# Optimization experiments

Measured on AMD Instinct MI355X. Metric: run time of the kernel, lower is better.

The kernel has to match this reference:

```python
import jax, jax.numpy as jnp
import numpy as np
from functools import partial

T = 2048        # num tokens
H = 2048        # hidden_size
I = 1024        # intermediate_size (per TP rank)
E = 8           # num_local_experts
TOP_K = 2       # num_experts_per_tok


def setup_inputs() -> dict:
    key = jax.random.key(0)
    k1, k2, k3, k4 = jax.random.split(key, 4)
    hidden_states = jax.random.normal(k1, (T, H), dtype=jnp.float32)
    gate_w = jax.random.normal(k2, (E, H), dtype=jnp.float32) * (H ** -0.5)
    # ws: [E, 2I, H] merged w1(gate)+w3(up); w2s: [E, H, I]
    ws = jax.random.normal(k3, (E, 2 * I, H), dtype=jnp.float32) * (H ** -0.5)
    w2s = jax.random.normal(k4, (E, H, I), dtype=jnp.float32) * (I ** -0.5)
    return {"hidden_states": hidden_states, "gate_w": gate_w, "ws": ws, "w2s": w2s}


def _moe_forward(x, gate_w, ws, w2s):
    num_tokens = x.shape[0]
    # router: replicated linear -> softmax -> top-k (fused_topk semantics)
    router_logits = x @ gate_w.T                     # [T, E]
    probs = jax.nn.softmax(router_logits, axis=-1)
    topk_weights, topk_ids = jax.lax.top_k(probs, TOP_K)   # [T, K]
    if TOP_K > 1:  # renormalize (do_normalize = top_k > 1)
        topk_weights = topk_weights / jnp.sum(topk_weights, axis=-1, keepdims=True)
    # combine weights as dense [T, E] (zero where expert not selected)
    cw = jnp.zeros((num_tokens, E), dtype=x.dtype)
    cw = cw.at[jnp.arange(num_tokens)[:, None], topk_ids].add(topk_weights)
    # grouped expert GEMMs; loop over the small fixed expert set
    out = jnp.zeros_like(x)
    for e in range(E):
        gate_up = x @ ws[e].T                        # [T, 2I]
        act = jax.nn.silu(gate_up[:, :I]) * gate_up[:, I:]  # SiluAndMul
        out = out + cw[:, e:e + 1] * (act @ w2s[e].T)       # [T, H]
    return out


def reference(hidden_states, gate_w, ws, w2s):
    return _moe_forward(hidden_states, gate_w, ws, w2s)
```

## Files before the change

### kernel.cpp

```cpp
#include <hip/hip_runtime.h>
#include <hip/hip_bf16.h>
#include <stdint.h>

#define TOKS  2048
#define HID   2048
#define ITR   1024
#define NEXP  8
#define NROWS 4096

typedef __attribute__((ext_vector_type(4))) float f32x4;
typedef __attribute__((ext_vector_type(8))) __bf16 bf16x8;
typedef __attribute__((ext_vector_type(8))) unsigned short u16x8;
typedef __attribute__((ext_vector_type(4))) unsigned short u16x4;

__device__ __forceinline__ unsigned short f2bf(float f) {
    union { float f; uint32_t u; } c; c.f = f;
    return (unsigned short)((c.u + 0x7FFFu + ((c.u >> 16) & 1u)) >> 16);
}

__device__ __forceinline__ void gll16(const unsigned short* g, unsigned short* l) {
    __builtin_amdgcn_global_load_lds(
        (const __attribute__((address_space(1))) unsigned int*)g,
        (__attribute__((address_space(3))) unsigned int*)l,
        16, 0, 0);
}

__global__ __launch_bounds__(256) void prep_kernel(const float* __restrict__ ws,
                                                   const float* __restrict__ w2s,
                                                   const float* __restrict__ x,
                                                   const float* __restrict__ gw,
                                                   float* __restrict__ out,
                                                   unsigned short* __restrict__ da,
                                                   unsigned short* __restrict__ db,
                                                   unsigned short* __restrict__ xb,
                                                   int* __restrict__ topk_id,
                                                   float* __restrict__ topk_w) {
    const int tid = threadIdx.x;

    if (tid < 64) {
        const int t = blockIdx.x;
        const int lane = tid;
        float acc[NEXP];
#pragma unroll
        for (int e = 0; e < NEXP; ++e) acc[e] = 0.f;
        const float* xr = x + (size_t)t * HID;
        unsigned short* xbr = xb + (size_t)t * HID;
        for (int s4 = lane; s4 < HID / 4; s4 += 64) {
            const f32x4 xv = *(const f32x4*)(xr + s4 * 4);
            u16x4 o;
#pragma unroll
            for (int j = 0; j < 4; ++j) o[j] = f2bf(xv[j]);
            *(u16x4*)(xbr + s4 * 4) = o;
#pragma unroll
            for (int e = 0; e < NEXP; ++e) {
                const f32x4 gv = *(const f32x4*)(gw + e * HID + s4 * 4);
                acc[e] += xv[0] * gv[0] + xv[1] * gv[1] + xv[2] * gv[2] + xv[3] * gv[3];
            }
        }
#pragma unroll
        for (int e = 0; e < NEXP; ++e) {
            float v = acc[e];
            for (int off = 32; off > 0; off >>= 1) v += __shfl_down(v, off, 64);
            acc[e] = v;
        }
        if (lane == 0) {
            float m0 = -1e30f, m1 = -1e30f; int i0 = 0, i1 = 0;
#pragma unroll
            for (int e = 0; e < NEXP; ++e) {
                float v = acc[e];
                if (v > m0) { m1 = m0; i1 = i0; m0 = v; i0 = e; }
                else if (v > m1) { m1 = v; i1 = e; }
            }
            float w0 = 1.f / (1.f + expf(m1 - m0));
            topk_id[t * 2] = i0; topk_id[t * 2 + 1] = i1;
            topk_w[t * 2] = w0;  topk_w[t * 2 + 1] = 1.f - w0;
        }
    }

    const int NA = (NEXP * 2 * ITR * HID) / 16;
    const int NB = (NEXP * HID * ITR) / 16;
    const int NO = (TOKS * HID) / 16;
    const int i0 = blockIdx.x * 256 + tid;
    const int stride = gridDim.x * 256;
    for (int k = i0; k < NA; k += stride) {
        const f32x4* p = (const f32x4*)(ws + (size_t)k * 16);
        f32x4 a = p[0], b = p[1], c = p[2], d = p[3];
        u16x8 o0, o1;
#pragma unroll
        for (int j = 0; j < 4; ++j) { o0[j] = f2bf(a[j]); o0[4 + j] = f2bf(b[j]); }
#pragma unroll
        for (int j = 0; j < 4; ++j) { o1[j] = f2bf(c[j]); o1[4 + j] = f2bf(d[j]); }
        *(u16x8*)(da + (size_t)k * 16) = o0;
        *(u16x8*)(da + (size_t)k * 16 + 8) = o1;
    }
    for (int k = i0; k < NB; k += stride) {
        const f32x4* p = (const f32x4*)(w2s + (size_t)k * 16);
        f32x4 a = p[0], b = p[1], c = p[2], d = p[3];
        u16x8 o0, o1;
#pragma unroll
        for (int j = 0; j < 4; ++j) { o0[j] = f2bf(a[j]); o0[4 + j] = f2bf(b[j]); }
#pragma unroll
        for (int j = 0; j < 4; ++j) { o1[j] = f2bf(c[j]); o1[4 + j] = f2bf(d[j]); }
        *(u16x8*)(db + (size_t)k * 16) = o0;
        *(u16x8*)(db + (size_t)k * 16 + 8) = o1;
    }
    const f32x4 z = (f32x4){0.f, 0.f, 0.f, 0.f};
    for (int k = i0; k < NO; k += stride) {
        f32x4* q = (f32x4*)(out + (size_t)k * 16);
        q[0] = z; q[1] = z; q[2] = z; q[3] = z;
    }
}

__global__ __launch_bounds__(512) void sort_kernel(const int* __restrict__ topk_id,
                                                   const float* __restrict__ topk_w,
                                                   int* __restrict__ sorted_tok,
                                                   float* __restrict__ row_w,
                                                   int* __restrict__ offsets,
                                                   int* __restrict__ counts) {
    __shared__ int sc[512 * NEXP];
    __shared__ int base[NEXP + 1];
    const int t = threadIdx.x;
    int ids[8];
    int* myrow = &sc[t * NEXP];
#pragma unroll
    for (int e = 0; e < NEXP; ++e) myrow[e] = 0;
#pragma unroll
    for (int j = 0; j < 8; ++j) { ids[j] = topk_id[t * 8 + j]; myrow[ids[j]]++; }
    __syncthreads();
    for (int d = 1; d < 512; d <<= 1) {
        int add[NEXP];
        const bool act = (t >= d);
#pragma unroll
        for (int e = 0; e < NEXP; ++e) add[e] = act ? sc[(t - d) * NEXP + e] : 0;
        __syncthreads();
        if (act) {
#pragma unroll
            for (int e = 0; e < NEXP; ++e) sc[t * NEXP + e] += add[e];
        }
        __syncthreads();
    }
    if (t == 0) {
        int s = 0;
        for (int e = 0; e < NEXP; ++e) {
            const int tot = sc[511 * NEXP + e];
            base[e] = s; offsets[e] = s; counts[e] = tot; s += tot;
        }
        base[NEXP] = s; offsets[NEXP] = s;
    }
    __syncthreads();
    int own[NEXP];
#pragma unroll
    for (int e = 0; e < NEXP; ++e) {
        int c = 0;
#pragma unroll
        for (int j = 0; j < 8; ++j) c += (ids[j] == e) ? 1 : 0;
        own[e] = c;
    }
#pragma unroll
    for (int e = 0; e < NEXP; ++e) myrow[e] = base[e] + myrow[e] - own[e];
#pragma unroll
    for (int j = 0; j < 8; ++j) {
        const int p = t * 8 + j;
        const int pos = myrow[ids[j]]++;
        sorted_tok[pos] = p >> 1;
        row_w[pos] = topk_w[p];
    }
}

__global__ __launch_bounds__(512) void gemm1_kernel(const unsigned short* __restrict__ Wb,
                                                    const unsigned short* __restrict__ Xb,
                                                    const int* __restrict__ offsets,
                                                    const int* __restrict__ counts,
                                                    const int* __restrict__ sorted_tok,
                                                    unsigned short* __restrict__ act) {
    const int b = blockIdx.x;
    const int e = b & 7;
    const int r = b >> 3;
    const int mt = r >> 4;
    const int nt = r & 15;
    const int cnt = counts[e];
    if (mt * 128 >= cnt) return;
    const int offs = offsets[e];
    const int tid = threadIdx.x, lane = tid & 63, wid = tid >> 6;
    const int wr = wid >> 2, wc = wid & 3;

    __shared__ unsigned short sA[3][128 * 32];
    __shared__ unsigned short sB[3][128 * 32];

    const int srow = tid >> 2;
    const int swz = (((tid & 3) ^ (srow & 3))) * 8;
    int ar = mt * 128 + srow;
    if (ar >= cnt) ar = cnt - 1;
    const int tok = sorted_tok[offs + ar];
    const unsigned short* aSrc = Xb + (size_t)tok * HID + swz;
    const unsigned short* wBase = Wb + (size_t)e * (2 * ITR) * HID;
    const int wrow = (srow < 64) ? (nt * 64 + srow) : (ITR + nt * 64 + (srow - 64));
    const unsigned short* bSrc = wBase + (size_t)wrow * HID + swz;
    const int ldsOff = wid * 16 * 32;

    f32x4 accg[4], accu[4];
#pragma unroll
    for (int i = 0; i < 4; ++i) {
        accg[i] = (f32x4){0.f, 0.f, 0.f, 0.f};
        accu[i] = (f32x4){0.f, 0.f, 0.f, 0.f};
    }

#define G1_STAGE(ks) do {                                  \
        const int k0_ = (ks) * 32;                         \
        gll16(aSrc + k0_, sA[(ks) % 3] + ldsOff);          \
        gll16(bSrc + k0_, sB[(ks) % 3] + ldsOff);          \
    } while (0)

    G1_STAGE(0);
    G1_STAGE(1);

    const int fr = lane & 15, fq = lane >> 4;
    const int sfo = (fq ^ (fr & 3)) * 8;
    const int NS = HID / 32;
    for (int ks = 0; ks < NS; ++ks) {
        const int cur = ks % 3;
        if (ks == NS - 1) asm volatile("s_waitcnt vmcnt(0)" ::: "memory");
        else              asm volatile("s_waitcnt vmcnt(2)" ::: "memory");
        __builtin_amdgcn_s_barrier();
        asm volatile("" ::: "memory");
        if (ks + 2 < NS) G1_STAGE(ks + 2);
        bf16x8 af[4], bg, bu;
#pragma unroll
        for (int mi = 0; mi < 4; ++mi)
            af[mi] = *(const bf16x8*)&sA[cur][(wr * 64 + mi * 16 + fr) * 32 + sfo];
        bg = *(const bf16x8*)&sB[cur][(wc * 16 + fr) * 32 + sfo];
        bu = *(const bf16x8*)&sB[cur][(64 + wc * 16 + fr) * 32 + sfo];
        __builtin_amdgcn_s_setprio(1);
#pragma unroll
        for (int mi = 0; mi < 4; ++mi) {
            accg[mi] = __builtin_amdgcn_mfma_f32_16x16x32_bf16(af[mi], bg, accg[mi], 0, 0, 0);
            accu[mi] = __builtin_amdgcn_mfma_f32_16x16x32_bf16(af[mi], bu, accu[mi], 0, 0, 0);
        }
        __builtin_amdgcn_s_setprio(0);
        asm volatile("" ::: "memory");
    }
#undef G1_STAGE

#pragma unroll
    for (int mi = 0; mi < 4; ++mi) {
#pragma unroll
        for (int j = 0; j < 4; ++j) {
            const int gr = mt * 128 + wr * 64 + mi * 16 + fq * 4 + j;
            if (gr < cnt) {
                const float g = accg[mi][j], u = accu[mi][j];
                const float s = g / (1.f + expf(-g));
                act[(size_t)(offs + gr) * ITR + nt * 64 + wc * 16 + fr] = f2bf(s * u);
            }
        }
    }
}

__global__ __launch_bounds__(512) void gemm2_kernel(const unsigned short* __restrict__ W2b,
                                                    const unsigned short* __restrict__ actb,
                                                    const int* __restrict__ offsets,
                                                    const int* __restrict__ counts,
                                                    const int* __restrict__ sorted_tok,
                                                    const float* __restrict__ row_w,
                                                    float* __restrict__ out) {
    const int b = blockIdx.x;
    const int e = b & 7;
    const int r = b >> 3;
    const int mt = r >> 4;
    const int nt = r & 15;
    const int cnt = counts[e];
    if (mt * 128 >= cnt) return;
    const int offs = offsets[e];
    const int tid = threadIdx.x, lane = tid & 63, wid = tid >> 6;
    const int wr = wid >> 2, wc = wid & 3;

    __shared__ unsigned short sA[3][128 * 32];
    __shared__ unsigned short sB[3][128 * 32];

    const int srow = tid >> 2;
    const int swz = (((tid & 3) ^ (srow & 3))) * 8;
    int ar = mt * 128 + srow;
    if (ar >= cnt) ar = cnt - 1;
    const unsigned short* aSrc = actb + (size_t)(offs + ar) * ITR + swz;
    const unsigned short* bSrc = W2b + ((size_t)e * HID + nt * 128 + srow) * ITR + swz;
    const int ldsOff = wid * 16 * 32;

    f32x4 acc[4][2];
#pragma unroll
    for (int i = 0; i < 4; ++i)
#pragma unroll
        for (int j = 0; j < 2; ++j) acc[i][j] = (f32x4){0.f, 0.f, 0.f, 0.f};

#define G2_STAGE(ks) do {                                  \
        const int k0_ = (ks) * 32;                         \
        gll16(aSrc + k0_, sA[(ks) % 3] + ldsOff);          \
        gll16(bSrc + k0_, sB[(ks) % 3] + ldsOff);          \
    } while (0)

    G2_STAGE(0);
    G2_STAGE(1);

    const int fr = lane & 15, fq = lane >> 4;
    const int sfo = (fq ^ (fr & 3)) * 8;
    const int NS = ITR / 32;
    for (int ks = 0; ks < NS; ++ks) {
        const int cur = ks % 3;
        if (ks == NS - 1) asm volatile("s_waitcnt vmcnt(0)" ::: "memory");
        else              asm volatile("s_waitcnt vmcnt(2)" ::: "memory");
        __builtin_amdgcn_s_barrier();
        asm volatile("" ::: "memory");
        if (ks + 2 < NS) G2_STAGE(ks + 2);
        bf16x8 af[4], bfv[2];
#pragma unroll
        for (int mi = 0; mi < 4; ++mi)
            af[mi] = *(const bf16x8*)&sA[cur][(wr * 64 + mi * 16 + fr) * 32 + sfo];
#pragma unroll
        for (int ni = 0; ni < 2; ++ni)
            bfv[ni] = *(const bf16x8*)&sB[cur][(wc * 32 + ni * 16 + fr) * 32 + sfo];
        __builtin_amdgcn_s_setprio(1);
#pragma unroll
        for (int mi = 0; mi < 4; ++mi)
#pragma unroll
            for (int ni = 0; ni < 2; ++ni)
                acc[mi][ni] = __builtin_amdgcn_mfma_f32_16x16x32_bf16(af[mi], bfv[ni], acc[mi][ni], 0, 0, 0);
        __builtin_amdgcn_s_setprio(0);
        asm volatile("" ::: "memory");
    }
#undef G2_STAGE

#pragma unroll
    for (int mi = 0; mi < 4; ++mi) {
#pragma unroll
        for (int j = 0; j < 4; ++j) {
            const int gr = mt * 128 + wr * 64 + mi * 16 + fq * 4 + j;
            if (gr < cnt) {
                const int pos = offs + gr;
                const int t = sorted_tok[pos];
                const float w = row_w[pos];
#pragma unroll
                for (int ni = 0; ni < 2; ++ni) {
                    const int col = nt * 128 + wc * 32 + ni * 16 + fr;
                    atomicAdd(&out[(size_t)t * HID + col], w * acc[mi][ni][j]);
                }
            }
        }
    }
}

extern "C" void kernel_launch(void* const* d_in, const int* in_sizes, int n_in,
                              void* d_out, int out_size, void* d_ws, size_t ws_size,
                              hipStream_t stream) {
    const float* x   = (const float*)d_in[0];
    const float* gw  = (const float*)d_in[1];
    const float* ws  = (const float*)d_in[2];
    const float* w2s = (const float*)d_in[3];
    float* out = (float*)d_out;

    char* wsb = (char*)d_ws;
    int*   counts     = (int*)(wsb + 0);
    int*   offsets    = (int*)(wsb + 256);
    int*   topk_id    = (int*)(wsb + 4096);
    float* topk_w     = (float*)(wsb + 20480);
    int*   sorted_tok = (int*)(wsb + 36864);
    float* row_w      = (float*)(wsb + 53248);
    unsigned short* xb    = (unsigned short*)(wsb + (1u << 20));
    unsigned short* actb  = (unsigned short*)(wsb + 9437184);
    unsigned short* wsb16 = (unsigned short*)(wsb + 17825792);
    unsigned short* w2b   = (unsigned short*)(wsb + 84934656);

    prep_kernel<<<2048, 256, 0, stream>>>(ws, w2s, x, gw, out, wsb16, w2b, xb, topk_id, topk_w);
    sort_kernel<<<1, 512, 0, stream>>>(topk_id, topk_w, sorted_tok, row_w, offsets, counts);
    gemm1_kernel<<<2048, 512, 0, stream>>>(wsb16, xb, offsets, counts, sorted_tok, actb);
    gemm2_kernel<<<2048, 512, 0, stream>>>(w2b, actb, offsets, counts, sorted_tok, row_w, out);
}
```

Before: 186.7 us.

## Move w2 bf16 conversion into idle gemm1 blocks and memset output

```diff
diff --git a/kernel.cpp b/kernel.cpp
--- a/kernel.cpp
+++ b/kernel.cpp
@@ -26,12 +26,9 @@
 }
 
 __global__ __launch_bounds__(256) void prep_kernel(const float* __restrict__ ws,
-                                                   const float* __restrict__ w2s,
                                                    const float* __restrict__ x,
                                                    const float* __restrict__ gw,
-                                                   float* __restrict__ out,
                                                    unsigned short* __restrict__ da,
-                                                   unsigned short* __restrict__ db,
                                                    unsigned short* __restrict__ xb,
                                                    int* __restrict__ topk_id,
                                                    float* __restrict__ topk_w) {
@@ -78,8 +75,6 @@
     }
 
     const int NA = (NEXP * 2 * ITR * HID) / 16;
-    const int NB = (NEXP * HID * ITR) / 16;
-    const int NO = (TOKS * HID) / 16;
     const int i0 = blockIdx.x * 256 + tid;
     const int stride = gridDim.x * 256;
     for (int k = i0; k < NA; k += stride) {
@@ -92,22 +87,6 @@
         for (int j = 0; j < 4; ++j) { o1[j] = f2bf(c[j]); o1[4 + j] = f2bf(d[j]); }
         *(u16x8*)(da + (size_t)k * 16) = o0;
         *(u16x8*)(da + (size_t)k * 16 + 8) = o1;
-    }
-    for (int k = i0; k < NB; k += stride) {
-        const f32x4* p = (const f32x4*)(w2s + (size_t)k * 16);
-        f32x4 a = p[0], b = p[1], c = p[2], d = p[3];
-        u16x8 o0, o1;
-#pragma unroll
-        for (int j = 0; j < 4; ++j) { o0[j] = f2bf(a[j]); o0[4 + j] = f2bf(b[j]); }
-#pragma unroll
-        for (int j = 0; j < 4; ++j) { o1[j] = f2bf(c[j]); o1[4 + j] = f2bf(d[j]); }
-        *(u16x8*)(db + (size_t)k * 16) = o0;
-        *(u16x8*)(db + (size_t)k * 16 + 8) = o1;
-    }
-    const f32x4 z = (f32x4){0.f, 0.f, 0.f, 0.f};
-    for (int k = i0; k < NO; k += stride) {
-        f32x4* q = (f32x4*)(out + (size_t)k * 16);
-        q[0] = z; q[1] = z; q[2] = z; q[3] = z;
     }
 }
 
@@ -169,6 +148,8 @@
 
 __global__ __launch_bounds__(512) void gemm1_kernel(const unsigned short* __restrict__ Wb,
                                                     const unsigned short* __restrict__ Xb,
+                                                    const float* __restrict__ w2s,
+                                                    unsigned short* __restrict__ w2b,
                                                     const int* __restrict__ offsets,
                                                     const int* __restrict__ counts,
                                                     const int* __restrict__ sorted_tok,
@@ -176,12 +157,31 @@
     const int b = blockIdx.x;
     const int e = b & 7;
     const int r = b >> 3;
+    const int tid = threadIdx.x;
+
+    if (r >= 128) {
+        const size_t base = ((size_t)((r - 128) << 3 | e)) * 16384;
+#pragma unroll
+        for (int it = 0; it < 2; ++it) {
+            const size_t k = base + (size_t)(it * 512 + tid) * 16;
+            const f32x4* p = (const f32x4*)(w2s + k);
+            f32x4 a = p[0], b2 = p[1], c = p[2], d = p[3];
+            u16x8 o0, o1;
+#pragma unroll
+            for (int j = 0; j < 4; ++j) { o0[j] = f2bf(a[j]); o0[4 + j] = f2bf(b2[j]); }
+#pragma unroll
+            for (int j = 0; j < 4; ++j) { o1[j] = f2bf(c[j]); o1[4 + j] = f2bf(d[j]); }
+            *(u16x8*)(w2b + k) = o0;
+            *(u16x8*)(w2b + k + 8) = o1;
+        }
+    }
+
     const int mt = r >> 4;
     const int nt = r & 15;
     const int cnt = counts[e];
     if (mt * 128 >= cnt) return;
     const int offs = offsets[e];
-    const int tid = threadIdx.x, lane = tid & 63, wid = tid >> 6;
+    const int lane = tid & 63, wid = tid >> 6;
     const int wr = wid >> 2, wc = wid & 3;
 
     __shared__ unsigned short sA[3][128 * 32];
@@ -367,8 +367,9 @@
     unsigned short* wsb16 = (unsigned short*)(wsb + 17825792);
     unsigned short* w2b   = (unsigned short*)(wsb + 84934656);
 
-    prep_kernel<<<2048, 256, 0, stream>>>(ws, w2s, x, gw, out, wsb16, w2b, xb, topk_id, topk_w);
+    hipMemsetAsync(out, 0, (size_t)out_size * sizeof(float), stream);
+    prep_kernel<<<2048, 256, 0, stream>>>(ws, x, gw, wsb16, xb, topk_id, topk_w);
     sort_kernel<<<1, 512, 0, stream>>>(topk_id, topk_w, sorted_tok, row_w, offsets, counts);
-    gemm1_kernel<<<2048, 512, 0, stream>>>(wsb16, xb, offsets, counts, sorted_tok, actb);
+    gemm1_kernel<<<2048, 512, 0, stream>>>(wsb16, xb, w2s, w2b, offsets, counts, sorted_tok, actb);
     gemm2_kernel<<<2048, 512, 0, stream>>>(w2b, actb, offsets, counts, sorted_tok, row_w, out);
 }
```

Result: no change. 188.3 us (+0.8%).
